# Kernel optimization log

Measured on AMD Instinct MI355X. Metric: run time of the kernel, lower is better.

The kernel has to match this reference:

```python
import jax, jax.numpy as jnp
import numpy as np
import math

MAX_SIZE = 2048  # max_size init arg


def setup_inputs() -> dict:
    key = jax.random.key(0)
    k1, k2, k3 = jax.random.split(key, 3)
    B, S, D = 16, 1024, 512
    PRED = 256
    data = jax.random.normal(k1, (B, S, D), dtype=jnp.float32)
    W = jax.random.normal(k2, (PRED, D), dtype=jnp.float32) * (1.0 / math.sqrt(D))
    b = jax.random.normal(k3, (PRED,), dtype=jnp.float32) * 0.01
    return {"data": data, "W": W, "b": b}


def reference(data, W, b):
    # data: [B, S, D]; self-attention with q=k=v=data
    B, S, D = data.shape
    pred_len = W.shape[0]
    scale = 1.0 / math.sqrt(D)
    scores = jnp.einsum('bsd,btd->bst', data, data) * scale          # [B,S,S]
    prob = jax.nn.softmax(scores, axis=-1)
    attn = jnp.einsum('bst,btd->bsd', prob, data)                     # [B,S,D]
    # NOTE: the original concatenates a 'mask' block (rows S..2S) onto attn,
    # but the per-timestep Linear loop only reads rows 0..S-1, so the mask
    # never affects the output (dead code). The loop collapses to one GEMM.
    lin = jnp.einsum('bsd,pd->bsp', attn, W) + b                      # [B,S,pred_len]
    out = jnp.zeros((B, MAX_SIZE, pred_len), dtype=data.dtype)
    out = out.at[:, :S, :].set(lin)
    return out
```

## Files before the change

kernel.cpp:

```cpp
#include <hip/hip_runtime.h>
#include <cstdint>
#include <cstddef>

#define B_    16
#define S_    1024
#define D_    512
#define P_    256
#define MAXS_ 2048

typedef unsigned short u16;
typedef unsigned int   u32;
typedef _Float16 f16;
typedef _Float16 f16x8 __attribute__((ext_vector_type(8)));
typedef float  f32x4  __attribute__((ext_vector_type(4)));
typedef unsigned short u16x4 __attribute__((ext_vector_type(4)));
typedef unsigned short u16x8 __attribute__((ext_vector_type(8)));

__device__ __forceinline__ void gld_lds16(const void* g, void* l) {
  __builtin_amdgcn_global_load_lds(
      (const __attribute__((address_space(1))) u32*)g,
      (__attribute__((address_space(3))) u32*)l, 16, 0, 0);
}

__device__ __forceinline__ u16 f2h(float f) {
  return __builtin_bit_cast(u16, (f16)f);
}
__device__ __forceinline__ float h2f(u16 h) {
  return (float)__builtin_bit_cast(f16, h);
}

template<int BPB>
__device__ __forceinline__ void xcd_map(int L, int& bz, int& r) {
  const int t = L & 7;
  const int j = L >> 3;
  bz = (t << 1) | (j / BPB);
  r  = j % BPB;
}

__global__ void convert_f16_kernel(const float* __restrict__ src, u16* __restrict__ dst, long n4) {
  long stride = (long)gridDim.x * blockDim.x;
  for (long i = (long)blockIdx.x * blockDim.x + threadIdx.x; i < n4; i += stride) {
    float4 v = ((const float4*)src)[i];
    u16x4 o;
    o[0] = f2h(v.x); o[1] = f2h(v.y); o[2] = f2h(v.z); o[3] = f2h(v.w);
    ((u16x4*)dst)[i] = o;
  }
}

__global__ __launch_bounds__(512, 2) void qk_pipe(
    const u16* __restrict__ A, u16* __restrict__ Cout,
    float2* __restrict__ rowpart, float scale) {
  extern __shared__ __align__(16) char smem[];
  const int tid  = threadIdx.x;
  const int lane = tid & 63;
  const int w    = tid >> 6;
  const int wm   = w >> 2;
  const int wn   = w & 3;
  const int lr   = lane & 15;
  const int hi   = lane >> 4;

  const int L = blockIdx.x + (blockIdx.y << 2) + (blockIdx.z << 4);
  int bz, r;
  xcd_map<16>(L, bz, r);
  const int I0 = (r >> 2) * 256;
  const int J0 = (r & 3) * 256;
  const u16* Ab = A + (long)bz * (S_ * D_);

  auto stageP = [&](int s, int part) {
    if (s >= 16) return;
    char* dst = smem + (s & 3) * 32768 + part * 16384;
    const int base = part ? J0 : I0;
    const int k0 = s * 32;
    #pragma unroll
    for (int i = 0; i < 2; ++i) {
      int cid   = i * 512 + tid;
      int inner = cid >> 2;
      int c     = (cid & 3) ^ ((inner >> 1) & 3);
      gld_lds16(Ab + (size_t)(base + inner) * D_ + k0 + c * 8, dst + cid * 16);
    }
  };

  f32x4 acc[8][4] = {};

  stageP(0, 0); stageP(0, 1);
  stageP(1, 0); stageP(1, 1);
  stageP(2, 0); stageP(2, 1);
  asm volatile("s_waitcnt vmcnt(8)" ::: "memory");
  __builtin_amdgcn_s_barrier();

  for (int s = 0; s < 16; ++s) {
    const char* sl = smem + (s & 3) * 32768;
    f16x8 bf[4];
    {
      f16x8 af[4];
      #pragma unroll
      for (int mq = 0; mq < 4; ++mq) {
        int row = wm * 128 + mq * 16 + lr;
        int cp  = hi ^ ((row >> 1) & 3);
        af[mq] = *(const f16x8*)(sl + row * 64 + cp * 16);
      }
      #pragma unroll
      for (int n = 0; n < 4; ++n) {
        int row = wn * 64 + n * 16 + lr;
        int cp  = hi ^ ((row >> 1) & 3);
        bf[n] = *(const f16x8*)(sl + 16384 + row * 64 + cp * 16);
      }
      stageP(s + 3, 0);
      __builtin_amdgcn_s_barrier();
      asm volatile("s_waitcnt lgkmcnt(0)" ::: "memory");
      __builtin_amdgcn_sched_barrier(0);
      __builtin_amdgcn_s_setprio(1);
      #pragma unroll
      for (int mq = 0; mq < 4; ++mq)
        #pragma unroll
        for (int n = 0; n < 4; ++n)
          acc[mq][n] = __builtin_amdgcn_mfma_f32_16x16x32_f16(af[mq], bf[n], acc[mq][n], 0, 0, 0);
      __builtin_amdgcn_s_setprio(0);
      __builtin_amdgcn_s_barrier();
    }
    {
      f16x8 af[4];
      #pragma unroll
      for (int mq = 0; mq < 4; ++mq) {
        int row = wm * 128 + 64 + mq * 16 + lr;
        int cp  = hi ^ ((row >> 1) & 3);
        af[mq] = *(const f16x8*)(sl + row * 64 + cp * 16);
      }
      stageP(s + 3, 1);
      __builtin_amdgcn_s_barrier();
      asm volatile("s_waitcnt lgkmcnt(0)" ::: "memory");
      __builtin_amdgcn_sched_barrier(0);
      __builtin_amdgcn_s_setprio(1);
      #pragma unroll
      for (int mq = 0; mq < 4; ++mq)
        #pragma unroll
        for (int n = 0; n < 4; ++n)
          acc[4 + mq][n] = __builtin_amdgcn_mfma_f32_16x16x32_f16(af[mq], bf[n], acc[4 + mq][n], 0, 0, 0);
      __builtin_amdgcn_s_setprio(0);
      if (s <= 12)      asm volatile("s_waitcnt vmcnt(8)" ::: "memory");
      else if (s == 13) asm volatile("s_waitcnt vmcnt(4)" ::: "memory");
      else if (s == 14) asm volatile("s_waitcnt vmcnt(0)" ::: "memory");
      __builtin_amdgcn_s_barrier();
    }
  }

  __syncthreads();
  float2* part = (float2*)smem;
  const float l2e = 1.4426950408889634f;
  u16* Cb = Cout + (long)bz * S_ * S_;
  const int row0 = I0 + wm * 128;
  const int col0 = J0 + wn * 64;
  #pragma unroll
  for (int m = 0; m < 8; ++m) {
    #pragma unroll
    for (int i = 0; i < 4; ++i) {
      int rr = row0 + m * 16 + (hi << 2) + i;
      float v[4];
      #pragma unroll
      for (int n = 0; n < 4; ++n) v[n] = acc[m][n][i] * scale;
      float mx = fmaxf(fmaxf(v[0], v[1]), fmaxf(v[2], v[3]));
      #pragma unroll
      for (int off = 1; off <= 8; off <<= 1)
        mx = fmaxf(mx, __shfl_xor(mx, off));
      float sum = 0.f;
      #pragma unroll
      for (int n = 0; n < 4; ++n) sum += exp2f((v[n] - mx) * l2e);
      #pragma unroll
      for (int off = 1; off <= 8; off <<= 1)
        sum += __shfl_xor(sum, off);
      #pragma unroll
      for (int n = 0; n < 4; ++n)
        Cb[(size_t)rr * S_ + col0 + n * 16 + lr] = f2h(v[n]);
      if (lr == 0)
        part[(wm * 128 + m * 16 + (hi << 2) + i) * 4 + wn] = make_float2(mx, sum);
    }
  }
  __syncthreads();
  if (tid < 256) {
    float2 a = part[tid * 4],     b = part[tid * 4 + 1];
    float2 c = part[tid * 4 + 2], d = part[tid * 4 + 3];
    float m = fmaxf(fmaxf(a.x, b.x), fmaxf(c.x, d.x));
    float l = a.y * exp2f((a.x - m) * l2e) + b.y * exp2f((b.x - m) * l2e)
            + c.y * exp2f((c.x - m) * l2e) + d.y * exp2f((d.x - m) * l2e);
    rowpart[((long)bz * 4 + (J0 >> 8)) * S_ + I0 + tid] = make_float2(m, l);
  }
}

__global__ __launch_bounds__(256, 2) void pv_slot(
    const u16* __restrict__ scores, const u16* __restrict__ VWT,
    const float2* __restrict__ rowpart,
    float* __restrict__ out, const float* __restrict__ bias) {
  extern __shared__ __align__(16) char smem[];
  const int tid  = threadIdx.x;
  const int lane = tid & 63;
  const int w    = tid >> 6;
  const int wm   = w >> 1;
  const int wn   = w & 1;
  const int lr   = lane & 15;
  const int hi   = lane >> 4;

  const int L = blockIdx.x + (blockIdx.y << 1) + (blockIdx.z << 6);
  int bz, rblk;
  xcd_map<64>(L, bz, rblk);
  const int yt = rblk >> 1;
  const int J0 = (rblk & 1) * 128;

  float* ob = out + (long)bz * MAXS_ * P_;
  if (yt >= 16) {
    f32x4 z = {0.f, 0.f, 0.f, 0.f};
    #pragma unroll 2
    for (int i = tid; i < 64 * 32; i += 256) {
      int rr = i >> 5;
      int c4 = i & 31;
      __builtin_nontemporal_store(z,
          (f32x4*)(ob + (size_t)(yt * 64 + rr) * P_ + J0) + c4);
    }
    return;
  }

  const int q0 = yt * 64;
  const u16* sA = scores + ((long)bz * S_ + q0) * S_;
  const u16* Vb = VWT + (long)bz * P_ * S_ + (size_t)J0 * S_;
  const float l2e = 1.4426950408889634f;

  const int ar0 = tid >> 3;
  const int ar1 = 32 + (tid >> 3);
  const int ac  = tid & 7;
  const int c0  = ac ^ (ar0 & 7);
  const int c1  = ac ^ (ar1 & 7);

  const float2* rp = rowpart + (long)bz * 4 * S_;
  auto mergeStat = [&](int row, float& nml, float& il) {
    float2 a = rp[row],          b = rp[S_ + row];
    float2 c = rp[2 * S_ + row], d = rp[3 * S_ + row];
    float m = fmaxf(fmaxf(a.x, b.x), fmaxf(c.x, d.x));
    float l = a.y * exp2f((a.x - m) * l2e) + b.y * exp2f((b.x - m) * l2e)
            + c.y * exp2f((c.x - m) * l2e) + d.y * exp2f((d.x - m) * l2e);
    nml = -m * l2e;
    il  = 1.f / l;
  };
  float nml0, il0, nml1, il1;
  mergeStat(q0 + ar0, nml0, il0);
  mergeStat(q0 + ar1, nml1, il1);

  auto loadA = [&](int s, u16x8 (&r)[2]) {
    r[0] = __builtin_nontemporal_load(
        (const u16x8*)(sA + (size_t)ar0 * S_ + s * 64 + c0 * 8));
    r[1] = __builtin_nontemporal_load(
        (const u16x8*)(sA + (size_t)ar1 * S_ + s * 64 + c1 * 8));
  };
  auto writeA = [&](int buf, u16x8 (&r)[2]) {
    char* dA = smem + buf * 8192;
    u16x8 p0, p1;
    #pragma unroll
    for (int j = 0; j < 8; ++j) {
      p0[j] = f2h(exp2f(fmaf(h2f(r[0][j]), l2e, nml0)) * il0);
      p1[j] = f2h(exp2f(fmaf(h2f(r[1][j]), l2e, nml1)) * il1);
    }
    *(u16x8*)(dA + (size_t)tid * 16)         = p0;
    *(u16x8*)(dA + (size_t)(256 + tid) * 16) = p1;
  };
  auto stageB = [&](int s, int buf) {
    char* dB = smem + 24576 + buf * 16384;
    #pragma unroll
    for (int i = 0; i < 4; ++i) {
      int cid = i * 256 + tid;
      int row = cid >> 3;
      int c   = (cid & 7) ^ (row & 7);
      gld_lds16(Vb + (size_t)row * S_ + s * 64 + c * 8, dB + cid * 16);
    }
  };

  f32x4 acc[2][4] = {};
  u16x8 rA[2][2];

  loadA(0, rA[0]);
  __builtin_amdgcn_sched_barrier(0);
  stageB(0, 0);
  __builtin_amdgcn_sched_barrier(0);
  loadA(1, rA[1]);
  __builtin_amdgcn_sched_barrier(0);
  stageB(1, 1);
  __builtin_amdgcn_sched_barrier(0);
  asm volatile("s_waitcnt vmcnt(6)" ::: "memory");
  writeA(0, rA[0]);
  asm volatile("s_waitcnt lgkmcnt(0)" ::: "memory");
  __builtin_amdgcn_s_barrier();

  #pragma unroll
  for (int s = 0; s < 16; ++s) {
    const int bufR = s % 3;
    const char* aB = smem + bufR * 8192;
    const char* bB = smem + 24576 + bufR * 16384;

    f16x8 af[2][2], bf[2][4];
    #pragma unroll
    for (int kk = 0; kk < 2; ++kk) {
      #pragma unroll
      for (int m = 0; m < 2; ++m) {
        int row = wm * 32 + m * 16 + lr;
        int cp  = (kk * 4 + hi) ^ (row & 7);
        af[kk][m] = *(const f16x8*)(aB + row * 128 + cp * 16);
      }
      #pragma unroll
      for (int n = 0; n < 4; ++n) {
        int row = wn * 64 + n * 16 + lr;
        int cp  = (kk * 4 + hi) ^ (row & 7);
        bf[kk][n] = *(const f16x8*)(bB + row * 128 + cp * 16);
      }
    }

    if (s + 2 < 16) {
      loadA(s + 2, rA[s & 1]);
      __builtin_amdgcn_sched_barrier(0);
      stageB(s + 2, (s + 2) % 3);
      __builtin_amdgcn_sched_barrier(0);
    }

    __builtin_amdgcn_s_setprio(1);
    #pragma unroll
    for (int kk = 0; kk < 2; ++kk)
      #pragma unroll
      for (int m = 0; m < 2; ++m)
        #pragma unroll
        for (int n = 0; n < 4; ++n)
          acc[m][n] = __builtin_amdgcn_mfma_f32_16x16x32_f16(
              af[kk][m], bf[kk][n], acc[m][n], 0, 0, 0);
    __builtin_amdgcn_s_setprio(0);

    if (s < 15) {
      if (s <= 13) asm volatile("s_waitcnt vmcnt(6)" ::: "memory");
      else         asm volatile("s_waitcnt vmcnt(0)" ::: "memory");
      writeA((s + 1) % 3, rA[(s + 1) & 1]);
      asm volatile("s_waitcnt lgkmcnt(0)" ::: "memory");
      __builtin_amdgcn_s_barrier();
    }
  }

  float bv[4];
  #pragma unroll
  for (int n = 0; n < 4; ++n) bv[n] = bias[J0 + wn * 64 + n * 16 + lr];
  #pragma unroll
  for (int m = 0; m < 2; ++m) {
    #pragma unroll
    for (int i = 0; i < 4; ++i) {
      int rr = q0 + wm * 32 + m * 16 + (hi << 2) + i;
      #pragma unroll
      for (int n = 0; n < 4; ++n)
        __builtin_nontemporal_store(acc[m][n][i] + bv[n],
            &ob[(size_t)rr * P_ + J0 + wn * 64 + n * 16 + lr]);
    }
  }
}

template<int KK, int BM, int BN, int NW, int WNS, int BPB>
__global__ __launch_bounds__(NW * 64, 2) void gemm_nt_small(
    const u16* __restrict__ A, const u16* __restrict__ Bm,
    u16* __restrict__ C, long sAb, long sBb, long sCb, int LDC) {
  constexpr int T   = NW * 64;
  constexpr int WMS = NW / WNS;
  constexpr int MF  = BM / (WMS * 16);
  constexpr int NF  = BN / (WNS * 16);
  constexpr int LA  = BM * 8 / T;
  constexpr int LB  = BN * 8 / T;
  constexpr int SZ  = (BM + BN) * 128;
  constexpr int NT  = KK / 64;

  extern __shared__ __align__(16) char smem[];
  const int tid  = threadIdx.x;
  const int lane = tid & 63;
  const int w    = tid >> 6;
  const int wm   = w / WNS;
  const int wn   = w % WNS;
  const int lr   = lane & 15;
  const int hi   = lane >> 4;

  const int L = blockIdx.x + gridDim.x * (blockIdx.y + gridDim.y * blockIdx.z);
  int bz, r;
  xcd_map<BPB>(L, bz, r);
  const int I0 = (r / gridDim.x) * BM;
  const int J0 = (r % gridDim.x) * BN;
  const u16* Ab = A  + (long)bz * sAb;
  const u16* Bb = Bm + (long)bz * sBb;

  auto stage = [&](int buf, int k0) {
    char* sA = smem + buf * SZ;
    char* sB = sA + BM * 128;
    #pragma unroll
    for (int i = 0; i < LA; ++i) {
      int cid = i * T + tid;
      int row = cid >> 3;
      int c   = (cid & 7) ^ (row & 7);
      gld_lds16(Ab + (size_t)(I0 + row) * KK + k0 + c * 8, sA + cid * 16);
    }
    #pragma unroll
    for (int i = 0; i < LB; ++i) {
      int cid = i * T + tid;
      int row = cid >> 3;
      int c   = (cid & 7) ^ (row & 7);
      gld_lds16(Bb + (size_t)(J0 + row) * KK + k0 + c * 8, sB + cid * 16);
    }
  };

  f32x4 acc[MF][NF] = {};
  stage(0, 0);
  for (int t = 0; t < NT; ++t) {
    const char* lA = smem + (t & 1) * SZ;
    const char* lB = lA + BM * 128;
    if (t + 1 < NT) {
      stage((t + 1) & 1, (t + 1) * 64);
      asm volatile("s_waitcnt vmcnt(%0)" :: "i"(LA + LB) : "memory");
    } else {
      asm volatile("s_waitcnt vmcnt(0)" ::: "memory");
    }
    __builtin_amdgcn_s_barrier();
    __builtin_amdgcn_sched_barrier(0);
    #pragma unroll
    for (int kk = 0; kk < 2; ++kk) {
      f16x8 af[MF], bfv[NF];
      #pragma unroll
      for (int m = 0; m < MF; ++m) {
        int row = wm * (MF * 16) + m * 16 + lr;
        int cp  = (kk * 4 + hi) ^ (row & 7);
        af[m] = *(const f16x8*)(lA + ((row * 8 + cp) << 4));
      }
      #pragma unroll
      for (int n = 0; n < NF; ++n) {
        int row = wn * (NF * 16) + n * 16 + lr;
        int cp  = (kk * 4 + hi) ^ (row & 7);
        bfv[n] = *(const f16x8*)(lB + ((row * 8 + cp) << 4));
      }
      __builtin_amdgcn_s_setprio(1);
      #pragma unroll
      for (int m = 0; m < MF; ++m)
        #pragma unroll
        for (int n = 0; n < NF; ++n)
          acc[m][n] = __builtin_amdgcn_mfma_f32_16x16x32_f16(af[m], bfv[n], acc[m][n], 0, 0, 0);
      __builtin_amdgcn_s_setprio(0);
    }
    __builtin_amdgcn_sched_barrier(0);
    __builtin_amdgcn_s_barrier();
  }

  const int row0 = I0 + wm * (MF * 16);
  const int col0 = J0 + wn * (NF * 16);
  #pragma unroll
  for (int m = 0; m < MF; ++m)
    #pragma unroll
    for (int i = 0; i < 4; ++i) {
      int rr = row0 + m * 16 + (hi << 2) + i;
      #pragma unroll
      for (int n = 0; n < NF; ++n)
        C[(long)bz * sCb + (size_t)rr * LDC + col0 + n * 16 + lr] = f2h(acc[m][n][i]);
    }
}

extern "C" void kernel_launch(void* const* d_in, const int* in_sizes, int n_in,
                              void* d_out, int out_size, void* d_ws, size_t ws_size,
                              hipStream_t stream) {
  const float* data = (const float*)d_in[0];
  const float* W    = (const float*)d_in[1];
  const float* bias = (const float*)d_in[2];
  float* out = (float*)d_out;
  char*  ws  = (char*)d_ws;

  const size_t MB = 1024 * 1024;
  u16*    dataH   = (u16*)(ws);
  u16*    Wh      = (u16*)(ws + 16 * MB);
  u16*    scoresH = (u16*)(ws + 17 * MB);
  u16*    VWT     = (u16*)(ws + 49 * MB);
  float2* rowpart = (float2*)(ws + 57 * MB);

  const float scale = 0.04419417382415922f;

  constexpr int SMEM_QK = 4 * 32768;
  constexpr int SMEM_PV = 3 * 8192 + 3 * 16384;
  constexpr int SMEM_VW = 2 * (64 + 128) * 128;

  (void)hipFuncSetAttribute((const void*)&qk_pipe,
                      hipFuncAttributeMaxDynamicSharedMemorySize, SMEM_QK);
  (void)hipFuncSetAttribute((const void*)&pv_slot,
                      hipFuncAttributeMaxDynamicSharedMemorySize, SMEM_PV);
  (void)hipFuncSetAttribute((const void*)&gemm_nt_small<512, 64, 128, 4, 2, 32>,
                      hipFuncAttributeMaxDynamicSharedMemorySize, SMEM_VW);

  convert_f16_kernel<<<2048, 256, 0, stream>>>(data, dataH, (long)B_ * S_ * D_ / 4);
  convert_f16_kernel<<<64, 256, 0, stream>>>(W, Wh, (long)P_ * D_ / 4);

  gemm_nt_small<512, 64, 128, 4, 2, 32><<<dim3(8, 4, 16), 256, SMEM_VW, stream>>>(
      Wh, dataH, VWT, 0L, (long)S_ * D_, (long)P_ * S_, S_);

  qk_pipe<<<dim3(4, 4, 16), 512, SMEM_QK, stream>>>(
      dataH, scoresH, rowpart, scale);

  pv_slot<<<dim3(2, 32, 16), 256, SMEM_PV, stream>>>(
      scoresH, VWT, rowpart, out, bias);
}
```

Baseline: 81.92 us.

## Merge split K-step phases into one and drop nontemporal hints

```diff
diff --git a/kernel.cpp b/kernel.cpp
--- a/kernel.cpp
+++ b/kernel.cpp
@@ -90,58 +90,45 @@
 
   for (int s = 0; s < 16; ++s) {
     const char* sl = smem + (s & 3) * 32768;
-    f16x8 bf[4];
-    {
-      f16x8 af[4];
-      #pragma unroll
-      for (int mq = 0; mq < 4; ++mq) {
-        int row = wm * 128 + mq * 16 + lr;
-        int cp  = hi ^ ((row >> 1) & 3);
-        af[mq] = *(const f16x8*)(sl + row * 64 + cp * 16);
-      }
-      #pragma unroll
-      for (int n = 0; n < 4; ++n) {
-        int row = wn * 64 + n * 16 + lr;
-        int cp  = hi ^ ((row >> 1) & 3);
-        bf[n] = *(const f16x8*)(sl + 16384 + row * 64 + cp * 16);
-      }
-      stageP(s + 3, 0);
-      __builtin_amdgcn_s_barrier();
-      asm volatile("s_waitcnt lgkmcnt(0)" ::: "memory");
-      __builtin_amdgcn_sched_barrier(0);
-      __builtin_amdgcn_s_setprio(1);
-      #pragma unroll
-      for (int mq = 0; mq < 4; ++mq)
-        #pragma unroll
-        for (int n = 0; n < 4; ++n)
-          acc[mq][n] = __builtin_amdgcn_mfma_f32_16x16x32_f16(af[mq], bf[n], acc[mq][n], 0, 0, 0);
-      __builtin_amdgcn_s_setprio(0);
-      __builtin_amdgcn_s_barrier();
-    }
-    {
-      f16x8 af[4];
-      #pragma unroll
-      for (int mq = 0; mq < 4; ++mq) {
-        int row = wm * 128 + 64 + mq * 16 + lr;
-        int cp  = hi ^ ((row >> 1) & 3);
-        af[mq] = *(const f16x8*)(sl + row * 64 + cp * 16);
-      }
-      stageP(s + 3, 1);
-      __builtin_amdgcn_s_barrier();
-      asm volatile("s_waitcnt lgkmcnt(0)" ::: "memory");
-      __builtin_amdgcn_sched_barrier(0);
-      __builtin_amdgcn_s_setprio(1);
-      #pragma unroll
-      for (int mq = 0; mq < 4; ++mq)
-        #pragma unroll
-        for (int n = 0; n < 4; ++n)
-          acc[4 + mq][n] = __builtin_amdgcn_mfma_f32_16x16x32_f16(af[mq], bf[n], acc[4 + mq][n], 0, 0, 0);
-      __builtin_amdgcn_s_setprio(0);
-      if (s <= 12)      asm volatile("s_waitcnt vmcnt(8)" ::: "memory");
-      else if (s == 13) asm volatile("s_waitcnt vmcnt(4)" ::: "memory");
-      else if (s == 14) asm volatile("s_waitcnt vmcnt(0)" ::: "memory");
-      __builtin_amdgcn_s_barrier();
-    }
+    f16x8 af0[4], af1[4], bf[4];
+    #pragma unroll
+    for (int mq = 0; mq < 4; ++mq) {
+      int row = wm * 128 + mq * 16 + lr;
+      int cp  = hi ^ ((row >> 1) & 3);
+      af0[mq] = *(const f16x8*)(sl + row * 64 + cp * 16);
+    }
+    #pragma unroll
+    for (int mq = 0; mq < 4; ++mq) {
+      int row = wm * 128 + 64 + mq * 16 + lr;
+      int cp  = hi ^ ((row >> 1) & 3);
+      af1[mq] = *(const f16x8*)(sl + row * 64 + cp * 16);
+    }
+    #pragma unroll
+    for (int n = 0; n < 4; ++n) {
+      int row = wn * 64 + n * 16 + lr;
+      int cp  = hi ^ ((row >> 1) & 3);
+      bf[n] = *(const f16x8*)(sl + 16384 + row * 64 + cp * 16);
+    }
+    stageP(s + 3, 0);
+    stageP(s + 3, 1);
+    asm volatile("s_waitcnt lgkmcnt(0)" ::: "memory");
+    __builtin_amdgcn_sched_barrier(0);
+    __builtin_amdgcn_s_setprio(1);
+    #pragma unroll
+    for (int mq = 0; mq < 4; ++mq)
+      #pragma unroll
+      for (int n = 0; n < 4; ++n)
+        acc[mq][n] = __builtin_amdgcn_mfma_f32_16x16x32_f16(af0[mq], bf[n], acc[mq][n], 0, 0, 0);
+    #pragma unroll
+    for (int mq = 0; mq < 4; ++mq)
+      #pragma unroll
+      for (int n = 0; n < 4; ++n)
+        acc[4 + mq][n] = __builtin_amdgcn_mfma_f32_16x16x32_f16(af1[mq], bf[n], acc[4 + mq][n], 0, 0, 0);
+    __builtin_amdgcn_s_setprio(0);
+    if (s <= 12)      asm volatile("s_waitcnt vmcnt(8)" ::: "memory");
+    else if (s == 13) asm volatile("s_waitcnt vmcnt(4)" ::: "memory");
+    else if (s == 14) asm volatile("s_waitcnt vmcnt(0)" ::: "memory");
+    __builtin_amdgcn_s_barrier();
   }
 
   __syncthreads();
@@ -207,13 +194,12 @@
 
   float* ob = out + (long)bz * MAXS_ * P_;
   if (yt >= 16) {
-    f32x4 z = {0.f, 0.f, 0.f, 0.f};
     #pragma unroll 2
     for (int i = tid; i < 64 * 32; i += 256) {
       int rr = i >> 5;
       int c4 = i & 31;
-      __builtin_nontemporal_store(z,
-          (f32x4*)(ob + (size_t)(yt * 64 + rr) * P_ + J0) + c4);
+      *((float4*)(ob + (size_t)(yt * 64 + rr) * P_ + J0) + c4) =
+          make_float4(0.f, 0.f, 0.f, 0.f);
     }
     return;
   }
@@ -244,10 +230,8 @@
   mergeStat(q0 + ar1, nml1, il1);
 
   auto loadA = [&](int s, u16x8 (&r)[2]) {
-    r[0] = __builtin_nontemporal_load(
-        (const u16x8*)(sA + (size_t)ar0 * S_ + s * 64 + c0 * 8));
-    r[1] = __builtin_nontemporal_load(
-        (const u16x8*)(sA + (size_t)ar1 * S_ + s * 64 + c1 * 8));
+    r[0] = *(const u16x8*)(sA + (size_t)ar0 * S_ + s * 64 + c0 * 8);
+    r[1] = *(const u16x8*)(sA + (size_t)ar1 * S_ + s * 64 + c1 * 8);
   };
   auto writeA = [&](int buf, u16x8 (&r)[2]) {
     char* dA = smem + buf * 8192;
@@ -347,8 +331,7 @@
       int rr = q0 + wm * 32 + m * 16 + (hi << 2) + i;
       #pragma unroll
       for (int n = 0; n < 4; ++n)
-        __builtin_nontemporal_store(acc[m][n][i] + bv[n],
-            &ob[(size_t)rr * P_ + J0 + wn * 64 + n * 16 + lr]);
+        ob[(size_t)rr * P_ + J0 + wn * 64 + n * 16 + lr] = acc[m][n][i] + bv[n];
     }
   }
 }
```

After: 78.39 us. 4.3% less time.
